# Optimization experiments

Measured on AMD Instinct MI355X. Metric: run time of the kernel, lower is better.

Reference implementation:

```python
import jax, jax.numpy as jnp
import numpy as np

B, T, C = 1, 2048, 1024
H, HKV, DH, WIN = 16, 4, 64, 128
EPS = 1e-5


def rotate_half(x):
    x1, x2 = jnp.split(x, 2, axis=-1)
    return jnp.concatenate((-x2, x1), axis=-1)


def setup_inputs() -> dict:
    key = jax.random.key(0)
    ks = jax.random.split(key, 8)
    s = 0.02
    return {
        "x": jax.random.normal(ks[0], (B, T, C), dtype=jnp.float32),
        "Wq": jax.random.normal(ks[1], (C, H * DH), dtype=jnp.float32) * s,
        "Wk": jax.random.normal(ks[2], (C, HKV * DH), dtype=jnp.float32) * s,
        "Wv": jax.random.normal(ks[3], (C, HKV * DH), dtype=jnp.float32) * s,
        "Wc": jax.random.normal(ks[4], (C, C), dtype=jnp.float32) * s,
        "Wg": jax.random.normal(ks[5], (C, H), dtype=jnp.float32) * s,
        "bg": jax.random.normal(ks[6], (H,), dtype=jnp.float32) * s,
        "rms_w": jnp.ones((C,), dtype=jnp.float32),
    }


def reference(x, Wq, Wk, Wv, Wc, Wg, bg, rms_w):
    n_rep = H // HKV
    # projections -> [B, heads, T, DH]
    q = (x @ Wq).reshape(B, T, H, DH).transpose(0, 2, 1, 3)
    k = (x @ Wk).reshape(B, T, HKV, DH).transpose(0, 2, 1, 3)
    v = (x @ Wv).reshape(B, T, HKV, DH).transpose(0, 2, 1, 3)
    # rotary embedding (freqs duplicated across the two halves)
    inv_freq = 1.0 / (10000.0 ** (jnp.arange(0, DH, 2, dtype=jnp.float32) / DH))
    freqs = jnp.arange(T, dtype=jnp.float32)[:, None] * inv_freq[None, :]
    emb = jnp.concatenate((freqs, freqs), axis=-1)  # [T, DH]
    cos, sin = jnp.cos(emb)[None, None], jnp.sin(emb)[None, None]
    q = q * cos + rotate_half(q) * sin
    k = k * cos + rotate_half(k) * sin
    # GQA: repeat kv heads (contiguous repeat matches torch expand+reshape)
    k = jnp.repeat(k, n_rep, axis=1)
    v = jnp.repeat(v, n_rep, axis=1)
    # gated decay
    gate_logits = (x @ Wg + bg).reshape(B, T, H, 1).transpose(0, 2, 1, 3)  # [B,H,T,1]
    log_alpha = jax.nn.log_sigmoid(gate_logits)
    log_in_scale = jax.nn.log_sigmoid(-gate_logits)
    k_scaled = k * jnp.exp(log_in_scale)
    la_cum = jnp.cumsum(log_alpha, axis=2)                  # [B,H,T,1]
    log_decay = la_cum - jnp.swapaxes(la_cum, 2, 3)         # [B,H,T,T]
    causal = jnp.triu(jnp.ones((T, T), dtype=bool), k=1)
    decay = jnp.exp(jnp.where(causal, -jnp.inf, log_decay))
    scores = jnp.einsum('bhtd,bhsd->bhts', q, k_scaled)
    y_global = jnp.einsum('bhts,bhsd->bhtd', scores * decay, v)
    nb = T // WIN
    qb = q.reshape(B, H, nb, WIN, DH)
    kb = k.reshape(B, H, nb, WIN, DH)
    vb = v.reshape(B, H, nb, WIN, DH)
    att = jnp.einsum('bhnqd,bhnkd->bhnqk', qb, kb) / jnp.sqrt(jnp.float32(DH))
    wmask = jnp.triu(jnp.ones((WIN, WIN), dtype=bool), k=1)
    att = jax.nn.softmax(jnp.where(wmask, -jnp.inf, att), axis=-1)
    y_local = jnp.einsum('bhnqk,bhnkd->bhnqd', att, vb).reshape(B, H, T, DH)
    # fuse, RMSNorm, output projection
    y = (y_global + y_local).transpose(0, 2, 1, 3).reshape(B, T, C)
    y = y * jax.lax.rsqrt(jnp.mean(y * y, axis=-1, keepdims=True) + EPS) * rms_w
    return y @ Wc
```

## Files before the change

kernel.cpp:

```cpp
#include <hip/hip_runtime.h>
#include <hip/hip_bf16.h>


typedef __attribute__((ext_vector_type(8))) short bf16x8;
typedef __attribute__((ext_vector_type(4))) float f32x4;

#define MFMA16(a, b, c) __builtin_amdgcn_mfma_f32_16x16x32_bf16(a, b, c, 0, 0, 0)
#define LN10000_OVER_32 0.28782313662425575f

__device__ __forceinline__ short f2b(float f) {
  __hip_bfloat16 h = __float2bfloat16(f);
  return *reinterpret_cast<short*>(&h);
}
__device__ __forceinline__ float b2f(short s) {
  return __uint_as_float(((unsigned)(unsigned short)s) << 16);
}
__device__ __forceinline__ void gload16(const void* g, void* l) {
  __builtin_amdgcn_global_load_lds(
      (const __attribute__((address_space(1))) void*)g,
      (__attribute__((address_space(3))) void*)l, 16, 0, 0);
}

__device__ __forceinline__ void transpose_cvt_body(
    const float* __restrict__ src, short* __restrict__ dst, int R, int C,
    int bx, int by, float* ts , const float* __restrict__ sw) {
  int c0 = bx * 32, r0 = by * 32;
  int tr = threadIdx.x >> 3, tc = (threadIdx.x & 7) * 4;
  float4 v = *(const float4*)&src[(size_t)(r0 + tr) * C + c0 + tc];
  ts[tr * 33 + tc] = v.x;
  ts[tr * 33 + tc + 1] = v.y;
  ts[tr * 33 + tc + 2] = v.z;
  ts[tr * 33 + tc + 3] = v.w;
  __syncthreads();
  alignas(8) short o[4];
#pragma unroll
  for (int i = 0; i < 4; ++i) {
    float m = sw ? sw[r0 + tc + i] : 1.0f;
    o[i] = f2b(ts[(tc + i) * 33 + tr] * m);
  }
  *(uint2*)&dst[(size_t)(c0 + tr) * R + r0 + tc] = *(uint2*)o;
}

__global__ __launch_bounds__(256) void prep_fused(
    const float* __restrict__ x, const float* __restrict__ Wq,
    const float* __restrict__ Wk, const float* __restrict__ Wv,
    const float* __restrict__ Wc, const float* __restrict__ Wg,
    const float* __restrict__ bg, const float* __restrict__ rmsw,
    short* __restrict__ xb, short* __restrict__ wqkvT,
    short* __restrict__ wcT, float* __restrict__ g, float* __restrict__ rs) {
  __shared__ float sbuf[2048 + 256];
  const int j = blockIdx.x;
  const int tid = threadIdx.x;
  if (j < 1024) {
    const int i = j * 2048 + tid * 8;
    float4 a = *(const float4*)(x + i);
    float4 b = *(const float4*)(x + i + 4);
    alignas(16) short o[8] = {f2b(a.x), f2b(a.y), f2b(a.z), f2b(a.w),
                              f2b(b.x), f2b(b.y), f2b(b.z), f2b(b.w)};
    *(float4*)(xb + i) = *(float4*)o;
    float* xs = sbuf;
    float* part = sbuf + 2048;
    *(float4*)(xs + tid * 8) = a;
    *(float4*)(xs + tid * 8 + 4) = b;
    __syncthreads();
    const int h = tid & 15, ch = (tid >> 4) & 7, row = tid >> 7;
    const float* xr = xs + row * 1024 + ch * 128;
    const float* wgp = Wg + (size_t)(ch * 128) * 16 + h;
    float acc = 0.f;
#pragma unroll 8
    for (int k = 0; k < 128; ++k) acc = fmaf(xr[k], wgp[k * 16], acc);
    part[row * 128 + ch * 16 + h] = acc;
    __syncthreads();
    if (tid < 32) {
      int rr = tid >> 4, hh = tid & 15;
      float s = bg[hh];
#pragma unroll
      for (int cc = 0; cc < 8; ++cc) s += part[rr * 128 + cc * 16 + hh];
      g[(j * 2 + rr) * 16 + hh] = s;
    }
  } else if (j < 2048) {
    int jj = j - 1024;
    transpose_cvt_body(Wq, wqkvT, 1024, 1024, jj & 31, jj >> 5, sbuf, nullptr);
  } else if (j < 2304) {
    int jj = j - 2048;
    transpose_cvt_body(Wk, wqkvT + 1024 * 1024, 1024, 256, jj & 7, jj >> 3,
                       sbuf, nullptr);
  } else if (j < 2560) {
    int jj = j - 2304;
    transpose_cvt_body(Wv, wqkvT + 1280 * 1024, 1024, 256, jj & 7, jj >> 3,
                       sbuf, nullptr);
  } else if (j < 3584) {
    int jj = j - 2560;
    transpose_cvt_body(Wc, wcT, 1024, 1024, jj & 31, jj >> 5, sbuf, rmsw);
  } else {
    int i4 = ((j - 3584) * 256 + tid) * 4;
    float4 z = {0.f, 0.f, 0.f, 0.f};
    *(float4*)(rs + i4) = z;
  }
}

__global__ __launch_bounds__(256) void qkv_gemm_fused(
    const short* __restrict__ A, const short* __restrict__ Bt,
    short* __restrict__ qkvb, short* __restrict__ vtb,
    short* __restrict__ ktb, const float* __restrict__ g,
    float* __restrict__ lac, float* __restrict__ insc) {
  __shared__ short As[128 * 64];
  __shared__ short Bs[64 * 64];
  __shared__ float part[256];
  const int id = blockIdx.x;
  const int tid = threadIdx.x;
  if (id >= 384) {
    const int h = id - 384;
    float vals[8];
    float local = 0.f;
#pragma unroll
    for (int i = 0; i < 8; ++i) {
      int t = tid * 8 + i;
      float gv = g[t * 16 + h];
      float la = (gv > 0.f) ? -log1pf(expf(-gv)) : (gv - log1pf(expf(gv)));
      insc[h * 2048 + t] = 1.f / (1.f + expf(gv));
      vals[i] = la;
      local += la;
    }
    part[tid] = local;
    __syncthreads();
    for (int off = 1; off < 256; off <<= 1) {
      float add = (tid >= off) ? part[tid - off] : 0.f;
      __syncthreads();
      part[tid] += add;
      __syncthreads();
    }
    float run = (tid > 0) ? part[tid - 1] : 0.f;
#pragma unroll
    for (int i = 0; i < 8; ++i) {
      run += vals[i];
      lac[h * 2048 + tid * 8 + i] = run;
    }
    return;
  }
  const int lane = tid & 63, wid = tid >> 6;
  const int l15 = lane & 15, lq = lane >> 4;
  const int jlin = id >> 3;
  const int by = (id & 7) + 8 * (jlin / 24);
  const int bx = jlin % 24;
  const int m0 = by * 128, n0 = bx * 64;
  const int K = 1024;
  const int srow = lane >> 3;
  const int sc16 = (lane & 7) ^ srow;
  f32x4 acc[2][4];
#pragma unroll
  for (int mt = 0; mt < 2; ++mt)
#pragma unroll
    for (int nt = 0; nt < 4; ++nt) acc[mt][nt] = {0.f, 0.f, 0.f, 0.f};
  for (int kt = 0; kt < K; kt += 64) {
    __syncthreads();
#pragma unroll
    for (int i = 0; i < 4; ++i) {
      int jj = wid * 4 + i;
      int row = jj * 8 + srow;
      gload16(A + (size_t)(m0 + row) * K + kt + sc16 * 8, &As[jj * 512]);
    }
#pragma unroll
    for (int i = 0; i < 2; ++i) {
      int jj = wid * 2 + i;
      int row = jj * 8 + srow;
      gload16(Bt + (size_t)(n0 + row) * K + kt + sc16 * 8, &Bs[jj * 512]);
    }
    __syncthreads();
    bf16x8 af[2][2], bfr[4][2];
#pragma unroll
    for (int ks = 0; ks < 2; ++ks) {
      int c16 = ks * 4 + lq;
#pragma unroll
      for (int mt = 0; mt < 2; ++mt) {
        int ar = wid * 32 + mt * 16 + l15;
        af[mt][ks] = *(const bf16x8*)&As[(ar * 8 + (c16 ^ (ar & 7))) * 8];
      }
#pragma unroll
      for (int nt = 0; nt < 4; ++nt) {
        int br = nt * 16 + l15;
        bfr[nt][ks] = *(const bf16x8*)&Bs[(br * 8 + (c16 ^ (br & 7))) * 8];
      }
    }
#pragma unroll
    for (int ks = 0; ks < 2; ++ks)
#pragma unroll
      for (int mt = 0; mt < 2; ++mt)
#pragma unroll
        for (int nt = 0; nt < 4; ++nt)
          acc[mt][nt] = MFMA16(af[mt][ks], bfr[nt][ks], acc[mt][nt]);
  }
  if (bx >= 20) {
#pragma unroll
    for (int mt = 0; mt < 2; ++mt) {
      int row0 = m0 + wid * 32 + mt * 16 + lq * 4;
#pragma unroll
      for (int nt = 0; nt < 4; ++nt) {
        int vcol = (n0 - 1280) + nt * 16 + l15;
        alignas(8) short o4[4];
#pragma unroll
        for (int r = 0; r < 4; ++r) o4[r] = f2b(acc[mt][nt][r]);
        *(uint2*)&vtb[(size_t)vcol * 2048 + row0] = *(uint2*)o4;
      }
    }
    return;
  }
  const bool isk = (bx >= 16);
#pragma unroll
  for (int mt = 0; mt < 2; ++mt) {
    int row0 = m0 + wid * 32 + mt * 16 + lq * 4;
#pragma unroll
    for (int nt = 0; nt < 2; ++nt) {
      int d = nt * 16 + l15;
      float ivf = __expf(-LN10000_OVER_32 * (float)d);
      alignas(8) short oa[4], ob[4];
#pragma unroll
      for (int r = 0; r < 4; ++r) {
        int row_g = row0 + r;
        float th = (float)row_g * ivf;
        float cs = cosf(th), sn = sinf(th);
        float a = acc[mt][nt][r], b = acc[mt][nt + 2][r];
        oa[r] = f2b(a * cs - b * sn);
        ob[r] = f2b(b * cs + a * sn);
        qkvb[(size_t)row_g * 1536 + n0 + d] = oa[r];
        qkvb[(size_t)row_g * 1536 + n0 + d + 32] = ob[r];
      }
      if (isk) {
        int dk = n0 - 1024 + d;
        *(uint2*)&ktb[(size_t)dk * 2048 + row0] = *(uint2*)oa;
        *(uint2*)&ktb[(size_t)(dk + 32) * 2048 + row0] = *(uint2*)ob;
      }
    }
  }
}

__global__ __launch_bounds__(256) void chunk_state(
    const short* __restrict__ vtb, const short* __restrict__ ktb,
    const float* __restrict__ lac, const float* __restrict__ insc,
    short* __restrict__ Bmat) {
  __shared__ short Ks[64 * 64], Vts[64 * 64];
  __shared__ float lacs[64], inss[64], gvals[64];
  const int tid = threadIdx.x, lane = tid & 63, wid = tid >> 6;
  const int l15 = lane & 15, lq = lane >> 4;
  const int h = blockIdx.y, kh = h >> 2, c = blockIdx.x;
  const int srow = lane >> 3;
  const int sc16 = (lane & 7) ^ srow;
#pragma unroll
  for (int i = 0; i < 2; ++i) {
    int jj = wid * 2 + i;
    int row = jj * 8 + srow;
    gload16(ktb + (size_t)(kh * 64 + row) * 2048 + c * 64 + sc16 * 8,
            &Ks[jj * 512]);
    gload16(vtb + (size_t)(kh * 64 + row) * 2048 + c * 64 + sc16 * 8,
            &Vts[jj * 512]);
  }
  if (tid < 64) {
    lacs[tid] = lac[h * 2048 + c * 64 + tid];
    inss[tid] = insc[h * 2048 + c * 64 + tid];
  }
  __syncthreads();
  if (tid < 64)
    gvals[tid] = __expf(fminf(lacs[63] - lacs[tid], 0.f)) * inss[tid];
  __syncthreads();
  const int er = wid * 16 + l15;
  bf16x8 av[2];
#pragma unroll
  for (int ks = 0; ks < 2; ++ks) {
    int c16 = ks * 4 + lq;
    bf16x8 raw = *(const bf16x8*)&Vts[(er * 8 + (c16 ^ (er & 7))) * 8];
    float4 g0 = *(const float4*)&gvals[c16 * 8];
    float4 g1 = *(const float4*)&gvals[c16 * 8 + 4];
    float gv[8] = {g0.x, g0.y, g0.z, g0.w, g1.x, g1.y, g1.z, g1.w};
    bf16x8 sc;
#pragma unroll
    for (int jx = 0; jx < 8; ++jx) sc[jx] = f2b(b2f(raw[jx]) * gv[jx]);
    av[ks] = sc;
  }
  f32x4 acc[4];
#pragma unroll
  for (int nt = 0; nt < 4; ++nt) acc[nt] = {0.f, 0.f, 0.f, 0.f};
#pragma unroll
  for (int ks = 0; ks < 2; ++ks) {
    int c16 = ks * 4 + lq;
#pragma unroll
    for (int nt = 0; nt < 4; ++nt) {
      int dr = nt * 16 + l15;
      bf16x8 bk = *(const bf16x8*)&Ks[(dr * 8 + (c16 ^ (dr & 7))) * 8];
      acc[nt] = MFMA16(av[ks], bk, acc[nt]);
    }
  }
  short* Bout = Bmat + (size_t)(h * 32 + c) * 4096;
#pragma unroll
  for (int nt = 0; nt < 4; ++nt)
#pragma unroll
    for (int r = 0; r < 4; ++r) {
      int e = wid * 16 + lq * 4 + r;
      Bout[e * 64 + nt * 16 + l15] = f2b(acc[nt][r]);
    }
}

__global__ __launch_bounds__(256) void scan_kernel(
    const short* __restrict__ Bmat, const float* __restrict__ lac,
    short* __restrict__ St) {
  const int h = blockIdx.x, sl = blockIdx.y, tid = threadIdx.x;
  __shared__ float lacE[32];
  if (tid < 32) lacE[tid] = lac[h * 2048 + tid * 64 + 63];
  __syncthreads();
  const int base = sl * 512 + tid * 2;
  float S0 = 0.f, S1 = 0.f;
  *(unsigned*)&St[(size_t)(h * 32) * 4096 + base] = 0u;
  unsigned p = *(const unsigned*)&Bmat[(size_t)(h * 32) * 4096 + base];
  for (int c = 1; c < 32; ++c) {
    unsigned n = p;
    if (c < 31)
      n = *(const unsigned*)&Bmat[(size_t)(h * 32 + c) * 4096 + base];
    float a = (c >= 2) ? __expf(fminf(lacE[c - 1] - lacE[c - 2], 0.f)) : 0.f;
    S0 = fmaf(a, S0, b2f((short)(p & 0xffffu)));
    S1 = fmaf(a, S1, b2f((short)(p >> 16)));
    unsigned pack = (unsigned)(unsigned short)f2b(S0) |
                    ((unsigned)(unsigned short)f2b(S1) << 16);
    *(unsigned*)&St[(size_t)(h * 32 + c) * 4096 + base] = pack;
    p = n;
  }
}

__global__ __launch_bounds__(256) void fused_attn(
    const short* __restrict__ qkv, const short* __restrict__ vtb,
    const short* __restrict__ St, const float* __restrict__ lac,
    const float* __restrict__ insc, short* __restrict__ ys,
    float* __restrict__ rs) {
  const int c = blockIdx.x, h = blockIdx.y;
  const int kh = h >> 2;
  const bool odd = (c & 1) != 0;
  __shared__ short Qs[64 * 64], Kd[64 * 64], Vd[64 * 64], Sts[64 * 64],
      Kp[64 * 64], Vp[64 * 64], Pd[64 * 64], Pp[64 * 64];
  __shared__ float lacq[64], inss[64];
  __shared__ float laprev_sh;
  const int tid = threadIdx.x, lane = tid & 63, wid = tid >> 6;
  const int l15 = lane & 15, lq = lane >> 4;
  const int srow = lane >> 3;
  const int sc16 = (lane & 7) ^ srow;
#pragma unroll
  for (int i = 0; i < 2; ++i) {
    int jj = wid * 2 + i;
    int row = jj * 8 + srow;
    gload16(qkv + (size_t)(c * 64 + row) * 1536 + h * 64 + sc16 * 8,
            &Qs[jj * 512]);
    gload16(qkv + (size_t)(c * 64 + row) * 1536 + 1024 + kh * 64 + sc16 * 8,
            &Kd[jj * 512]);
    gload16(vtb + (size_t)(kh * 64 + row) * 2048 + c * 64 + sc16 * 8,
            &Vd[jj * 512]);
    gload16(St + (size_t)(h * 32 + c) * 4096 + row * 64 + sc16 * 8,
            &Sts[jj * 512]);
  }
  if (odd) {
#pragma unroll
    for (int i = 0; i < 2; ++i) {
      int jj = wid * 2 + i;
      int row = jj * 8 + srow;
      gload16(qkv + (size_t)((c - 1) * 64 + row) * 1536 + 1024 + kh * 64 +
                  sc16 * 8,
              &Kp[jj * 512]);
      gload16(vtb + (size_t)(kh * 64 + row) * 2048 + (c - 1) * 64 + sc16 * 8,
              &Vp[jj * 512]);
    }
  }
  if (tid < 64) {
    lacq[tid] = lac[h * 2048 + c * 64 + tid];
    inss[tid] = insc[h * 2048 + c * 64 + tid];
  }
  if (tid == 0) laprev_sh = (c > 0) ? lac[h * 2048 + c * 64 - 1] : 1e30f;
  __syncthreads();
  const int qr = wid * 16 + l15;
  bf16x8 aq[2];
#pragma unroll
  for (int ks = 0; ks < 2; ++ks) {
    int c16 = ks * 4 + lq;
    aq[ks] = *(const bf16x8*)&Qs[(qr * 8 + (c16 ^ (qr & 7))) * 8];
  }
  f32x4 sv[4];
#pragma unroll
  for (int nt = 0; nt < 4; ++nt) {
    int kr = nt * 16 + l15;
    bf16x8 bk0 = *(const bf16x8*)&Kd[(kr * 8 + ((0 + lq) ^ (kr & 7))) * 8];
    bf16x8 bk1 = *(const bf16x8*)&Kd[(kr * 8 + ((4 + lq) ^ (kr & 7))) * 8];
    f32x4 z = {0.f, 0.f, 0.f, 0.f};
    z = MFMA16(aq[0], bk0, z);
    z = MFMA16(aq[1], bk1, z);
    sv[nt] = z;
  }
  f32x4 sp[4];
  if (odd) {
#pragma unroll
    for (int nt = 0; nt < 4; ++nt) {
      int kr = nt * 16 + l15;
      bf16x8 bk0 = *(const bf16x8*)&Kp[(kr * 8 + ((0 + lq) ^ (kr & 7))) * 8];
      bf16x8 bk1 = *(const bf16x8*)&Kp[(kr * 8 + ((4 + lq) ^ (kr & 7))) * 8];
      f32x4 z = {0.f, 0.f, 0.f, 0.f};
      z = MFMA16(aq[0], bk0, z);
      z = MFMA16(aq[1], bk1, z);
      sp[nt] = z;
    }
  } else {
#pragma unroll
    for (int nt = 0; nt < 4; ++nt) sp[nt] = {0.f, 0.f, 0.f, 0.f};
  }
  f32x4 oi[4];
#pragma unroll
  for (int nt = 0; nt < 4; ++nt) {
    int er = nt * 16 + l15;
    bf16x8 bs0 = *(const bf16x8*)&Sts[(er * 8 + ((0 + lq) ^ (er & 7))) * 8];
    bf16x8 bs1 = *(const bf16x8*)&Sts[(er * 8 + ((4 + lq) ^ (er & 7))) * 8];
    f32x4 z = {0.f, 0.f, 0.f, 0.f};
    z = MFMA16(aq[0], bs0, z);
    z = MFMA16(aq[1], bs1, z);
    oi[nt] = z;
  }
  float mrow[4], ssum[4];
  float vd[4][4], vp[4][4];
#pragma unroll
  for (int r = 0; r < 4; ++r) mrow[r] = -1e30f;
#pragma unroll
  for (int nt = 0; nt < 4; ++nt) {
    int col = nt * 16 + l15;
#pragma unroll
    for (int r = 0; r < 4; ++r) {
      int row = wid * 16 + lq * 4 + r;
      float xv = (col <= row) ? sv[nt][r] * 0.125f : -1e30f;
      vd[nt][r] = xv;
      mrow[r] = fmaxf(mrow[r], xv);
      if (odd) {
        float xp = sp[nt][r] * 0.125f;
        vp[nt][r] = xp;
        mrow[r] = fmaxf(mrow[r], xp);
      }
    }
  }
#pragma unroll
  for (int r = 0; r < 4; ++r) {
    for (int off = 1; off < 16; off <<= 1)
      mrow[r] = fmaxf(mrow[r], __shfl_xor(mrow[r], off, 64));
    ssum[r] = 0.f;
  }
#pragma unroll
  for (int nt = 0; nt < 4; ++nt) {
#pragma unroll
    for (int r = 0; r < 4; ++r) {
      float e = __expf(vd[nt][r] - mrow[r]);
      vd[nt][r] = e;
      ssum[r] += e;
      if (odd) {
        float ep = __expf(vp[nt][r] - mrow[r]);
        vp[nt][r] = ep;
        ssum[r] += ep;
      }
    }
  }
#pragma unroll
  for (int r = 0; r < 4; ++r) {
    for (int off = 1; off < 16; off <<= 1) ssum[r] += __shfl_xor(ssum[r], off, 64);
    ssum[r] = 1.f / ssum[r];
  }
#pragma unroll
  for (int nt = 0; nt < 4; ++nt) {
    int col = nt * 16 + l15;
    float ls = lacq[col], is = inss[col];
#pragma unroll
    for (int r = 0; r < 4; ++r) {
      int row = wid * 16 + lq * 4 + r;
      float w = __expf(fminf(lacq[row] - ls, 0.f)) * is;
      if (col > row) w = 0.f;
      float pc = sv[nt][r] * w + vd[nt][r] * ssum[r];
      Pd[(row * 8 + ((col >> 3) ^ (row & 7))) * 8 + (col & 7)] = f2b(pc);
      if (odd)
        Pp[(row * 8 + ((col >> 3) ^ (row & 7))) * 8 + (col & 7)] =
            f2b(vp[nt][r] * ssum[r]);
    }
  }
  __syncthreads();
  bf16x8 ap[2];
#pragma unroll
  for (int ks = 0; ks < 2; ++ks) {
    int c16 = ks * 4 + lq;
    ap[ks] = *(const bf16x8*)&Pd[(qr * 8 + (c16 ^ (qr & 7))) * 8];
  }
  f32x4 o[4];
#pragma unroll
  for (int nt = 0; nt < 4; ++nt) {
    int vr = nt * 16 + l15;
    bf16x8 bv0 = *(const bf16x8*)&Vd[(vr * 8 + ((0 + lq) ^ (vr & 7))) * 8];
    bf16x8 bv1 = *(const bf16x8*)&Vd[(vr * 8 + ((4 + lq) ^ (vr & 7))) * 8];
    f32x4 z = {0.f, 0.f, 0.f, 0.f};
    z = MFMA16(ap[0], bv0, z);
    z = MFMA16(ap[1], bv1, z);
    o[nt] = z;
  }
  if (odd) {
    bf16x8 app[2];
#pragma unroll
    for (int ks = 0; ks < 2; ++ks) {
      int c16 = ks * 4 + lq;
      app[ks] = *(const bf16x8*)&Pp[(qr * 8 + (c16 ^ (qr & 7))) * 8];
    }
#pragma unroll
    for (int nt = 0; nt < 4; ++nt) {
      int vr = nt * 16 + l15;
      bf16x8 bv0 = *(const bf16x8*)&Vp[(vr * 8 + ((0 + lq) ^ (vr & 7))) * 8];
      bf16x8 bv1 = *(const bf16x8*)&Vp[(vr * 8 + ((4 + lq) ^ (vr & 7))) * 8];
      o[nt] = MFMA16(app[0], bv0, o[nt]);
      o[nt] = MFMA16(app[1], bv1, o[nt]);
    }
  }
  const float laprev = laprev_sh;
#pragma unroll
  for (int r = 0; r < 4; ++r) {
    int row = wid * 16 + lq * 4 + r;
    float rfac = __expf(fminf(lacq[row] - laprev, 0.f));
    int row_g = c * 64 + row;
    float ssq = 0.f;
#pragma unroll
    for (int nt = 0; nt < 4; ++nt) {
      int colg = h * 64 + nt * 16 + l15;
      size_t idx = (size_t)row_g * 1024 + colg;
      float v = o[nt][r] + rfac * oi[nt][r];
      ys[idx] = f2b(v);
      ssq = fmaf(v, v, ssq);
    }
    for (int off = 1; off < 16; off <<= 1) ssq += __shfl_xor(ssq, off, 64);
    if (l15 == 0) atomicAdd(&rs[row_g], ssq);
  }
}

__global__ __launch_bounds__(256) void out_gemm(
    const short* __restrict__ A, const short* __restrict__ Bt,
    const float* __restrict__ rs, float* __restrict__ C) {
  __shared__ short As[64 * 64];
  __shared__ short Bs[64 * 64];
  const int tid = threadIdx.x, lane = tid & 63, wid = tid >> 6;
  const int l15 = lane & 15, lq = lane >> 4;
  const int wm = wid >> 1, wn = wid & 1;
  const int id = blockIdx.x;
  const int jlin = id >> 3;
  const int by = (id & 7) + 8 * (jlin / 16);
  const int bx = jlin % 16;
  const int m0 = by * 64, n0 = bx * 64;
  const int K = 1024;
  const int srow = lane >> 3;
  const int sc16 = (lane & 7) ^ srow;
  f32x4 acc[2][2];
#pragma unroll
  for (int mt = 0; mt < 2; ++mt)
#pragma unroll
    for (int nt = 0; nt < 2; ++nt) acc[mt][nt] = {0.f, 0.f, 0.f, 0.f};
  for (int kt = 0; kt < K; kt += 64) {
    __syncthreads();
#pragma unroll
    for (int i = 0; i < 2; ++i) {
      int jj = wid * 2 + i;
      int row = jj * 8 + srow;
      gload16(A + (size_t)(m0 + row) * K + kt + sc16 * 8, &As[jj * 512]);
      gload16(Bt + (size_t)(n0 + row) * K + kt + sc16 * 8, &Bs[jj * 512]);
    }
    __syncthreads();
    bf16x8 af[2][2], bfr[2][2];
#pragma unroll
    for (int ks = 0; ks < 2; ++ks) {
      int c16 = ks * 4 + lq;
#pragma unroll
      for (int mt = 0; mt < 2; ++mt) {
        int ar = wm * 32 + mt * 16 + l15;
        af[mt][ks] = *(const bf16x8*)&As[(ar * 8 + (c16 ^ (ar & 7))) * 8];
      }
#pragma unroll
      for (int nt = 0; nt < 2; ++nt) {
        int br = wn * 32 + nt * 16 + l15;
        bfr[nt][ks] = *(const bf16x8*)&Bs[(br * 8 + (c16 ^ (br & 7))) * 8];
      }
    }
#pragma unroll
    for (int ks = 0; ks < 2; ++ks)
#pragma unroll
      for (int mt = 0; mt < 2; ++mt)
#pragma unroll
        for (int nt = 0; nt < 2; ++nt)
          acc[mt][nt] = MFMA16(af[mt][ks], bfr[nt][ks], acc[mt][nt]);
  }
#pragma unroll
  for (int mt = 0; mt < 2; ++mt) {
    int row0 = m0 + wm * 32 + mt * 16 + lq * 4;
#pragma unroll
    for (int r = 0; r < 4; ++r) {
      int row_g = row0 + r;
      float sc = rsqrtf(rs[row_g] * (1.0f / 1024.0f) + 1e-5f);
#pragma unroll
      for (int nt = 0; nt < 2; ++nt)
        C[(size_t)row_g * 1024 + n0 + wn * 32 + nt * 16 + l15] =
            acc[mt][nt][r] * sc;
    }
  }
}

extern "C" void kernel_launch(void* const* d_in, const int* in_sizes, int n_in,
                              void* d_out, int out_size, void* d_ws,
                              size_t ws_size, hipStream_t stream) {
  const float* x = (const float*)d_in[0];
  const float* Wq = (const float*)d_in[1];
  const float* Wk = (const float*)d_in[2];
  const float* Wv = (const float*)d_in[3];
  const float* Wc = (const float*)d_in[4];
  const float* Wg = (const float*)d_in[5];
  const float* bg = (const float*)d_in[6];
  const float* rmsw = (const float*)d_in[7];
  float* out = (float*)d_out;

  short* wqkvT = (short*)d_ws;
  short* wcT = wqkvT + 1536 * 1024;
  short* qkvb = wcT + 1024 * 1024;
  short* vtb = qkvb + 2048 * 1536;
  short* ktb = vtb + 256 * 2048;
  float* gw = (float*)(ktb + 256 * 2048);
  float* lacw = gw + 2048 * 16;
  float* inscw = lacw + 16 * 2048;
  short* Bmat = (short*)(inscw + 16 * 2048);
  short* Stb = Bmat + 16 * 32 * 4096;
  short* xb = Stb + 16 * 32 * 4096;
  short* ys = xb;
  float* rsq = (float*)(xb + 2048 * 1024);

  prep_fused<<<3586, 256, 0, stream>>>(x, Wq, Wk, Wv, Wc, Wg, bg, rmsw, xb,
                                       wqkvT, wcT, gw, rsq);
  qkv_gemm_fused<<<400, 256, 0, stream>>>(xb, wqkvT, qkvb, vtb, ktb, gw, lacw,
                                          inscw);
  chunk_state<<<dim3(32, 16), 256, 0, stream>>>(vtb, ktb, lacw, inscw, Bmat);
  scan_kernel<<<dim3(16, 8), 256, 0, stream>>>(Bmat, lacw, Stb);
  fused_attn<<<dim3(32, 16), 256, 0, stream>>>(qkvb, vtb, Stb, lacw, inscw,
                                               ys, rsq);
  out_gemm<<<512, 256, 0, stream>>>(ys, wcT, rsq, out);
}
```

Before: 128.4 us.

## Fuse chunk-state computation and decay scan into one per-head kernel

Merges the per-chunk K^T·(gated V) state kernel and the separate scan kernel into a single kernel with one block per head. That block walks the 32 chunks serially, double-buffers the next chunk's K/V tiles into LDS, and carries the running state in fp32 registers. This removes one launch and the round trip of the intermediate Bmat buffer through global memory. In exchange, parallelism drops from 512 blocks to 16, so the work becomes a latency-bound serial chain of 31 steps, each with a barrier and a global load.

```diff
diff --git a/kernel.cpp b/kernel.cpp
--- a/kernel.cpp
+++ b/kernel.cpp
@@ -234,93 +234,91 @@
   }
 }
 
-__global__ __launch_bounds__(256) void chunk_state(
+__global__ __launch_bounds__(256) void chunk_scan(
     const short* __restrict__ vtb, const short* __restrict__ ktb,
     const float* __restrict__ lac, const float* __restrict__ insc,
-    short* __restrict__ Bmat) {
-  __shared__ short Ks[64 * 64], Vts[64 * 64];
-  __shared__ float lacs[64], inss[64], gvals[64];
+    short* __restrict__ St) {
+  const int h = blockIdx.x, kh = h >> 2;
+  __shared__ short Ks[2][4096], Vts[2][4096];
+  __shared__ float gvs[2048];
+  __shared__ float lacE[32];
   const int tid = threadIdx.x, lane = tid & 63, wid = tid >> 6;
   const int l15 = lane & 15, lq = lane >> 4;
-  const int h = blockIdx.y, kh = h >> 2, c = blockIdx.x;
   const int srow = lane >> 3;
   const int sc16 = (lane & 7) ^ srow;
+  for (int i = tid; i < 2048; i += 256) {
+    float la = lac[h * 2048 + i];
+    float laE = lac[h * 2048 + (i | 63)];
+    gvs[i] = __expf(fminf(laE - la, 0.f)) * insc[h * 2048 + i];
+  }
+  if (tid < 32) lacE[tid] = lac[h * 2048 + tid * 64 + 63];
+  {
+    short* s0 = St + (size_t)(h * 32) * 4096;
+    alignas(16) short z8[8] = {0, 0, 0, 0, 0, 0, 0, 0};
+    *(uint4*)&s0[tid * 16] = *(uint4*)z8;
+    *(uint4*)&s0[tid * 16 + 8] = *(uint4*)z8;
+  }
 #pragma unroll
   for (int i = 0; i < 2; ++i) {
     int jj = wid * 2 + i;
     int row = jj * 8 + srow;
-    gload16(ktb + (size_t)(kh * 64 + row) * 2048 + c * 64 + sc16 * 8,
-            &Ks[jj * 512]);
-    gload16(vtb + (size_t)(kh * 64 + row) * 2048 + c * 64 + sc16 * 8,
-            &Vts[jj * 512]);
-  }
-  if (tid < 64) {
-    lacs[tid] = lac[h * 2048 + c * 64 + tid];
-    inss[tid] = insc[h * 2048 + c * 64 + tid];
-  }
-  __syncthreads();
-  if (tid < 64)
-    gvals[tid] = __expf(fminf(lacs[63] - lacs[tid], 0.f)) * inss[tid];
-  __syncthreads();
-  const int er = wid * 16 + l15;
-  bf16x8 av[2];
-#pragma unroll
-  for (int ks = 0; ks < 2; ++ks) {
-    int c16 = ks * 4 + lq;
-    bf16x8 raw = *(const bf16x8*)&Vts[(er * 8 + (c16 ^ (er & 7))) * 8];
-    float4 g0 = *(const float4*)&gvals[c16 * 8];
-    float4 g1 = *(const float4*)&gvals[c16 * 8 + 4];
-    float gv[8] = {g0.x, g0.y, g0.z, g0.w, g1.x, g1.y, g1.z, g1.w};
-    bf16x8 sc;
-#pragma unroll
-    for (int jx = 0; jx < 8; ++jx) sc[jx] = f2b(b2f(raw[jx]) * gv[jx]);
-    av[ks] = sc;
-  }
-  f32x4 acc[4];
-#pragma unroll
-  for (int nt = 0; nt < 4; ++nt) acc[nt] = {0.f, 0.f, 0.f, 0.f};
-#pragma unroll
-  for (int ks = 0; ks < 2; ++ks) {
-    int c16 = ks * 4 + lq;
-#pragma unroll
-    for (int nt = 0; nt < 4; ++nt) {
-      int dr = nt * 16 + l15;
-      bf16x8 bk = *(const bf16x8*)&Ks[(dr * 8 + (c16 ^ (dr & 7))) * 8];
-      acc[nt] = MFMA16(av[ks], bk, acc[nt]);
-    }
-  }
-  short* Bout = Bmat + (size_t)(h * 32 + c) * 4096;
-#pragma unroll
-  for (int nt = 0; nt < 4; ++nt)
-#pragma unroll
-    for (int r = 0; r < 4; ++r) {
-      int e = wid * 16 + lq * 4 + r;
-      Bout[e * 64 + nt * 16 + l15] = f2b(acc[nt][r]);
-    }
-}
-
-__global__ __launch_bounds__(256) void scan_kernel(
-    const short* __restrict__ Bmat, const float* __restrict__ lac,
-    short* __restrict__ St) {
-  const int h = blockIdx.x, sl = blockIdx.y, tid = threadIdx.x;
-  __shared__ float lacE[32];
-  if (tid < 32) lacE[tid] = lac[h * 2048 + tid * 64 + 63];
-  __syncthreads();
-  const int base = sl * 512 + tid * 2;
-  float S0 = 0.f, S1 = 0.f;
-  *(unsigned*)&St[(size_t)(h * 32) * 4096 + base] = 0u;
-  unsigned p = *(const unsigned*)&Bmat[(size_t)(h * 32) * 4096 + base];
-  for (int c = 1; c < 32; ++c) {
-    unsigned n = p;
-    if (c < 31)
-      n = *(const unsigned*)&Bmat[(size_t)(h * 32 + c) * 4096 + base];
-    float a = (c >= 2) ? __expf(fminf(lacE[c - 1] - lacE[c - 2], 0.f)) : 0.f;
-    S0 = fmaf(a, S0, b2f((short)(p & 0xffffu)));
-    S1 = fmaf(a, S1, b2f((short)(p >> 16)));
-    unsigned pack = (unsigned)(unsigned short)f2b(S0) |
-                    ((unsigned)(unsigned short)f2b(S1) << 16);
-    *(unsigned*)&St[(size_t)(h * 32 + c) * 4096 + base] = pack;
-    p = n;
+    gload16(ktb + (size_t)(kh * 64 + row) * 2048 + sc16 * 8, &Ks[0][jj * 512]);
+    gload16(vtb + (size_t)(kh * 64 + row) * 2048 + sc16 * 8, &Vts[0][jj * 512]);
+  }
+  f32x4 S[4];
+#pragma unroll
+  for (int nt = 0; nt < 4; ++nt) S[nt] = {0.f, 0.f, 0.f, 0.f};
+  int cur = 0;
+  for (int c = 0; c < 31; ++c) {
+    __syncthreads();
+    if (c < 30) {
+      int nc = c + 1;
+#pragma unroll
+      for (int i = 0; i < 2; ++i) {
+        int jj = wid * 2 + i;
+        int row = jj * 8 + srow;
+        gload16(ktb + (size_t)(kh * 64 + row) * 2048 + nc * 64 + sc16 * 8,
+                &Ks[cur ^ 1][jj * 512]);
+        gload16(vtb + (size_t)(kh * 64 + row) * 2048 + nc * 64 + sc16 * 8,
+                &Vts[cur ^ 1][jj * 512]);
+      }
+    }
+    const int er = wid * 16 + l15;
+    bf16x8 av[2];
+#pragma unroll
+    for (int ks = 0; ks < 2; ++ks) {
+      int c16 = ks * 4 + lq;
+      bf16x8 raw = *(const bf16x8*)&Vts[cur][(er * 8 + (c16 ^ (er & 7))) * 8];
+      bf16x8 sc;
+#pragma unroll
+      for (int jx = 0; jx < 8; ++jx)
+        sc[jx] = f2b(b2f(raw[jx]) * gvs[c * 64 + c16 * 8 + jx]);
+      av[ks] = sc;
+    }
+    f32x4 bacc[4];
+#pragma unroll
+    for (int nt = 0; nt < 4; ++nt) bacc[nt] = {0.f, 0.f, 0.f, 0.f};
+#pragma unroll
+    for (int ks = 0; ks < 2; ++ks) {
+      int c16 = ks * 4 + lq;
+#pragma unroll
+      for (int nt = 0; nt < 4; ++nt) {
+        int dr = nt * 16 + l15;
+        bf16x8 bk = *(const bf16x8*)&Ks[cur][(dr * 8 + (c16 ^ (dr & 7))) * 8];
+        bacc[nt] = MFMA16(av[ks], bk, bacc[nt]);
+      }
+    }
+    const float a = (c >= 1) ? __expf(fminf(lacE[c] - lacE[c - 1], 0.f)) : 0.f;
+    short* So = St + (size_t)(h * 32 + c + 1) * 4096;
+#pragma unroll
+    for (int nt = 0; nt < 4; ++nt)
+#pragma unroll
+      for (int r = 0; r < 4; ++r) {
+        S[nt][r] = fmaf(a, S[nt][r], bacc[nt][r]);
+        int e = wid * 16 + lq * 4 + r;
+        So[e * 64 + nt * 16 + l15] = f2b(S[nt][r]);
+      }
+    cur ^= 1;
   }
 }
 
@@ -631,8 +629,7 @@
                                        wqkvT, wcT, gw, rsq);
   qkv_gemm_fused<<<400, 256, 0, stream>>>(xb, wqkvT, qkvb, vtb, ktb, gw, lacw,
                                           inscw);
-  chunk_state<<<dim3(32, 16), 256, 0, stream>>>(vtb, ktb, lacw, inscw, Bmat);
-  scan_kernel<<<dim3(16, 8), 256, 0, stream>>>(Bmat, lacw, Stb);
+  chunk_scan<<<16, 256, 0, stream>>>(vtb, ktb, lacw, inscw, Stb);
   fused_attn<<<dim3(32, 16), 256, 0, stream>>>(qkvb, vtb, Stb, lacw, inscw,
                                                ys, rsq);
   out_gemm<<<512, 256, 0, stream>>>(ys, wcT, rsq, out);
```

Result: slower. 155.4 us (+21.0%).

## Move Wc transpose and rs zeroing into the scan kernel launch

Applied to the files above, without the earlier changes.

Moves the Wc transpose/convert (with RMSNorm weight folding) and the zeroing of the row-sum buffer out of the prep kernel and into the scan kernel's launch as extra blocks. The scan kernel previously launched only 128 blocks and left most of the GPU idle, so the independent Wc work now fills that idle capacity and shortens the prep kernel on the critical path. The trade-off is that the scan blocks share the launch with about a thousand transpose blocks, which could delay the scan if it is scheduled behind them.

```diff
diff --git a/kernel.cpp b/kernel.cpp
--- a/kernel.cpp
+++ b/kernel.cpp
@@ -44,10 +44,9 @@
 __global__ __launch_bounds__(256) void prep_fused(
     const float* __restrict__ x, const float* __restrict__ Wq,
     const float* __restrict__ Wk, const float* __restrict__ Wv,
-    const float* __restrict__ Wc, const float* __restrict__ Wg,
-    const float* __restrict__ bg, const float* __restrict__ rmsw,
+    const float* __restrict__ Wg, const float* __restrict__ bg,
     short* __restrict__ xb, short* __restrict__ wqkvT,
-    short* __restrict__ wcT, float* __restrict__ g, float* __restrict__ rs) {
+    float* __restrict__ g) {
   __shared__ float sbuf[2048 + 256];
   const int j = blockIdx.x;
   const int tid = threadIdx.x;
@@ -85,17 +84,10 @@
     int jj = j - 2048;
     transpose_cvt_body(Wk, wqkvT + 1024 * 1024, 1024, 256, jj & 7, jj >> 3,
                        sbuf, nullptr);
-  } else if (j < 2560) {
+  } else {
     int jj = j - 2304;
     transpose_cvt_body(Wv, wqkvT + 1280 * 1024, 1024, 256, jj & 7, jj >> 3,
                        sbuf, nullptr);
-  } else if (j < 3584) {
-    int jj = j - 2560;
-    transpose_cvt_body(Wc, wcT, 1024, 1024, jj & 31, jj >> 5, sbuf, rmsw);
-  } else {
-    int i4 = ((j - 3584) * 256 + tid) * 4;
-    float4 z = {0.f, 0.f, 0.f, 0.f};
-    *(float4*)(rs + i4) = z;
   }
 }
 
@@ -299,28 +291,41 @@
     }
 }
 
-__global__ __launch_bounds__(256) void scan_kernel(
+__global__ __launch_bounds__(256) void scan_wc(
     const short* __restrict__ Bmat, const float* __restrict__ lac,
-    short* __restrict__ St) {
-  const int h = blockIdx.x, sl = blockIdx.y, tid = threadIdx.x;
-  __shared__ float lacE[32];
-  if (tid < 32) lacE[tid] = lac[h * 2048 + tid * 64 + 63];
-  __syncthreads();
-  const int base = sl * 512 + tid * 2;
-  float S0 = 0.f, S1 = 0.f;
-  *(unsigned*)&St[(size_t)(h * 32) * 4096 + base] = 0u;
-  unsigned p = *(const unsigned*)&Bmat[(size_t)(h * 32) * 4096 + base];
-  for (int c = 1; c < 32; ++c) {
-    unsigned n = p;
-    if (c < 31)
-      n = *(const unsigned*)&Bmat[(size_t)(h * 32 + c) * 4096 + base];
-    float a = (c >= 2) ? __expf(fminf(lacE[c - 1] - lacE[c - 2], 0.f)) : 0.f;
-    S0 = fmaf(a, S0, b2f((short)(p & 0xffffu)));
-    S1 = fmaf(a, S1, b2f((short)(p >> 16)));
-    unsigned pack = (unsigned)(unsigned short)f2b(S0) |
-                    ((unsigned)(unsigned short)f2b(S1) << 16);
-    *(unsigned*)&St[(size_t)(h * 32 + c) * 4096 + base] = pack;
-    p = n;
+    short* __restrict__ St, const float* __restrict__ Wc,
+    const float* __restrict__ rmsw, short* __restrict__ wcT,
+    float* __restrict__ rs) {
+  __shared__ float sbuf[1056];
+  const int bid = blockIdx.x, tid = threadIdx.x;
+  if (bid < 128) {
+    const int h = bid >> 3, sl = bid & 7;
+    float* lacE = sbuf;
+    if (tid < 32) lacE[tid] = lac[h * 2048 + tid * 64 + 63];
+    __syncthreads();
+    const int base = sl * 512 + tid * 2;
+    float S0 = 0.f, S1 = 0.f;
+    *(unsigned*)&St[(size_t)(h * 32) * 4096 + base] = 0u;
+    unsigned p = *(const unsigned*)&Bmat[(size_t)(h * 32) * 4096 + base];
+    for (int c = 1; c < 32; ++c) {
+      unsigned n = p;
+      if (c < 31)
+        n = *(const unsigned*)&Bmat[(size_t)(h * 32 + c) * 4096 + base];
+      float a = (c >= 2) ? __expf(fminf(lacE[c - 1] - lacE[c - 2], 0.f)) : 0.f;
+      S0 = fmaf(a, S0, b2f((short)(p & 0xffffu)));
+      S1 = fmaf(a, S1, b2f((short)(p >> 16)));
+      unsigned pack = (unsigned)(unsigned short)f2b(S0) |
+                      ((unsigned)(unsigned short)f2b(S1) << 16);
+      *(unsigned*)&St[(size_t)(h * 32 + c) * 4096 + base] = pack;
+      p = n;
+    }
+  } else if (bid < 1152) {
+    int jj = bid - 128;
+    transpose_cvt_body(Wc, wcT, 1024, 1024, jj & 31, jj >> 5, sbuf, rmsw);
+  } else {
+    int i4 = ((bid - 1152) * 256 + tid) * 4;
+    float4 z = {0.f, 0.f, 0.f, 0.f};
+    *(float4*)(rs + i4) = z;
   }
 }
 
@@ -627,12 +632,11 @@
   short* ys = xb;
   float* rsq = (float*)(xb + 2048 * 1024);
 
-  prep_fused<<<3586, 256, 0, stream>>>(x, Wq, Wk, Wv, Wc, Wg, bg, rmsw, xb,
-                                       wqkvT, wcT, gw, rsq);
+  prep_fused<<<2560, 256, 0, stream>>>(x, Wq, Wk, Wv, Wg, bg, xb, wqkvT, gw);
   qkv_gemm_fused<<<400, 256, 0, stream>>>(xb, wqkvT, qkvb, vtb, ktb, gw, lacw,
                                           inscw);
   chunk_state<<<dim3(32, 16), 256, 0, stream>>>(vtb, ktb, lacw, inscw, Bmat);
-  scan_kernel<<<dim3(16, 8), 256, 0, stream>>>(Bmat, lacw, Stb);
+  scan_wc<<<1154, 256, 0, stream>>>(Bmat, lacw, Stb, Wc, rmsw, wcT, rsq);
   fused_attn<<<dim3(32, 16), 256, 0, stream>>>(qkvb, vtb, Stb, lacw, inscw,
                                                ys, rsq);
   out_gemm<<<512, 256, 0, stream>>>(ys, wcT, rsq, out);
```

Result: slower. 133.3 us (+3.8%).
